# Optimization experiments

Hardware: AMD Instinct MI355X
Metric: run time of the kernel (lower is better)

Reference implementation:

```python
import jax, jax.numpy as jnp
import numpy as np


def setup_inputs() -> dict:
    key = jax.random.key(0)
    ks = jax.random.split(key, 5)
    B, S, D, U = 4, 2048, 1024, 1024
    scale = 1.0 / np.sqrt(D)
    return {
        "query": jax.random.normal(ks[0], (B, S, D), dtype=jnp.float32),
        "value": jax.random.normal(ks[1], (B, S, D), dtype=jnp.float32),
        "Wq": jax.random.normal(ks[2], (D, U), dtype=jnp.float32) * scale,
        "bq": jnp.zeros((U,), dtype=jnp.float32),
        "Wk": jax.random.normal(ks[3], (D, U), dtype=jnp.float32) * scale,
        "bk": jnp.zeros((U,), dtype=jnp.float32),
        "Wv": jax.random.normal(ks[4], (D, U), dtype=jnp.float32) * scale,
        "bv": jnp.zeros((U,), dtype=jnp.float32),
    }


def reference(query, value, Wq, bq, Wk, bk, Wv, bv):
    # Dense projections (last-dim matmul + bias)
    Q = jnp.einsum("bsd,du->bsu", query, Wq) + bq   # [B,Sq,U]
    K = jnp.einsum("btd,du->btu", value, Wk) + bk   # [B,Sk,U]
    V = jnp.einsum("btd,du->btu", value, Wv) + bv   # [B,Sk,U]
    d_k = jnp.asarray(K.shape[-1], dtype=jnp.float32)
    scores = jnp.einsum("bsu,btu->bst", Q, K) / jnp.sqrt(d_k)  # [B,Sq,Sk]
    weights = jax.nn.softmax(scores, axis=-1)
    return jnp.einsum("bst,btu->bsu", weights, V)   # [B,Sq,U]
```

## Files before the change

kernel.cpp:

```cpp
#include <hip/hip_runtime.h>
#include <hip/hip_bf16.h>
#include <stdint.h>

#define DEVINL __device__ __forceinline__

typedef __attribute__((ext_vector_type(4))) float f32x4;
typedef __attribute__((ext_vector_type(8))) __bf16 bfv8;
typedef __attribute__((ext_vector_type(8))) short s16x8;
typedef __attribute__((ext_vector_type(4))) short s16x4;

DEVINL short f2bf(float f) {
  union { float f; unsigned u; } v; v.f = f;
  unsigned r = v.u + 0x7FFFu + ((v.u >> 16) & 1u);
  return (short)(r >> 16);
}
DEVINL float bf2f(short h) {
  union { unsigned u; float f; } v; v.u = ((unsigned)(unsigned short)h) << 16;
  return v.f;
}
DEVINL void gload_lds16(const void* g, void* l) {
  __builtin_amdgcn_global_load_lds((__attribute__((address_space(1))) unsigned*)(g),
                                   (__attribute__((address_space(3))) unsigned*)(l),
                                   16, 0, 0);
}
#define S_BARRIER() __builtin_amdgcn_s_barrier()
#define LGKM0() asm volatile("s_waitcnt lgkmcnt(0)" ::: "memory")
#define MEMORD() asm volatile("" ::: "memory")
template <int N> DEVINL void vmwaitc() {
  asm volatile("s_waitcnt vmcnt(%0)" :: "i"(N) : "memory");
}

template <int BU, int NF>
DEVINL void gemm_core(const short* __restrict__ Ag, const short* __restrict__ Bg,
                      int lda, int ldb, int m0, int n0, int nkt,
                      short* lds, f32x4 (&acc)[8][NF]) {
  constexpr int U = 2 + BU;
  constexpr int SLOT = 8192 + BU * 4096;
  const int tid = threadIdx.x;
  const int w = tid >> 6, l = tid & 63;
  const int wm = w >> 2, wn = w & 3;
  const int lr = l & 15, lg = l >> 4;
  const int stg_row = w * 16 + (l >> 2);
  const int stg_col = (((l & 3) ^ ((l >> 3) & 3)) << 3);
  const int ck = ((lg ^ ((lr >> 1) & 3)) << 3);
  const int aro = (wm * 128 + lr) * 32 + ck;
  const int bro = 8192 + (wn * (NF * 16) + lr) * 32 + ck;
  const int dW = w * 512;

#pragma unroll
  for (int t = 0; t < 3; ++t) {
    short* S = lds + t * SLOT;
    gload_lds16(Ag + (size_t)(m0 + stg_row) * lda + t * 32 + stg_col, S + dW);
    gload_lds16(Ag + (size_t)(m0 + 128 + stg_row) * lda + t * 32 + stg_col, S + 4096 + dW);
#pragma unroll
    for (int u = 0; u < BU; ++u)
      gload_lds16(Bg + (size_t)(n0 + u * 128 + stg_row) * ldb + t * 32 + stg_col,
                  S + 8192 + u * 4096 + dW);
  }
  vmwaitc<2 * U>(); S_BARRIER(); MEMORD();

  bfv8 a[4], b[NF];
#pragma unroll 1
  for (int kt = 0; kt < nkt; ++kt) {
    const short* Sc = lds + (kt & 3) * SLOT;
    const int ks = kt + 3;
    short* Ss = lds + (ks & 3) * SLOT;
#pragma unroll
    for (int mf = 0; mf < 4; ++mf) a[mf] = *(const bfv8*)(Sc + aro + mf * 512);
#pragma unroll
    for (int nf = 0; nf < NF; ++nf) b[nf] = *(const bfv8*)(Sc + bro + nf * 512);
    if (ks < nkt) {
      gload_lds16(Ag + (size_t)(m0 + stg_row) * lda + ks * 32 + stg_col, Ss + dW);
      gload_lds16(Ag + (size_t)(m0 + 128 + stg_row) * lda + ks * 32 + stg_col, Ss + 4096 + dW);
    }
    S_BARRIER(); LGKM0();
    __builtin_amdgcn_s_setprio(1);
#pragma unroll
    for (int mf = 0; mf < 4; ++mf)
#pragma unroll
      for (int nf = 0; nf < NF; ++nf)
        acc[mf][nf] = __builtin_amdgcn_mfma_f32_16x16x32_bf16(a[mf], b[nf], acc[mf][nf], 0, 0, 0);
    __builtin_amdgcn_s_setprio(0);
    S_BARRIER(); MEMORD();
#pragma unroll
    for (int mf = 0; mf < 4; ++mf) a[mf] = *(const bfv8*)(Sc + aro + 2048 + mf * 512);
    if (ks < nkt) {
#pragma unroll
      for (int u = 0; u < BU; ++u)
        gload_lds16(Bg + (size_t)(n0 + u * 128 + stg_row) * ldb + ks * 32 + stg_col,
                    Ss + 8192 + u * 4096 + dW);
    }
    if (kt + 1 < nkt) {
      if (ks < nkt) vmwaitc<2 * U>();
      else if (kt + 2 < nkt) vmwaitc<U>();
      else vmwaitc<0>();
    }
    S_BARRIER(); LGKM0();
    __builtin_amdgcn_s_setprio(1);
#pragma unroll
    for (int mf = 0; mf < 4; ++mf)
#pragma unroll
      for (int nf = 0; nf < NF; ++nf)
        acc[4 + mf][nf] = __builtin_amdgcn_mfma_f32_16x16x32_bf16(a[mf], b[nf], acc[4 + mf][nf], 0, 0, 0);
    __builtin_amdgcn_s_setprio(0);
    S_BARRIER(); MEMORD();
  }
}

__global__ __launch_bounds__(256) void prep_kernel(
    const float* __restrict__ q, const float* __restrict__ v,
    const float* __restrict__ Wq, const float* __restrict__ Wk, const float* __restrict__ Wv,
    short* __restrict__ Qc, short* __restrict__ Vc,
    short* __restrict__ WTq, short* __restrict__ WTk, short* __restrict__ WTv) {
  __shared__ float tile[64][65];
  const int bx = blockIdx.x;
  if (bx < 8192) {
    const float* src = (bx < 4096) ? q : v;
    short* dst = (bx < 4096) ? Qc : Vc;
    const size_t i = ((size_t)(bx & 4095) * 256 + threadIdx.x) * 8;
    f32x4 x0 = *(const f32x4*)(src + i);
    f32x4 x1 = *(const f32x4*)(src + i + 4);
    s16x8 o;
#pragma unroll
    for (int j = 0; j < 4; ++j) { o[j] = f2bf(x0[j]); o[4 + j] = f2bf(x1[j]); }
    *(s16x8*)(dst + i) = o;
  } else {
    const int z = (bx - 8192) >> 8, xx = (bx - 8192) & 255;
    const float* W = (z == 0) ? Wq : (z == 1) ? Wk : Wv;
    short* WT = (z == 0) ? WTq : (z == 1) ? WTk : WTv;
    const int k0 = (xx & 15) << 6, n0 = (xx >> 4) << 6;
    const int c = threadIdx.x & 63, r0 = threadIdx.x >> 6;
#pragma unroll
    for (int i = 0; i < 16; ++i) {
      int r = (i << 2) + r0;
      tile[r][c] = W[(size_t)(k0 + r) * 1024 + n0 + c];
    }
    __syncthreads();
#pragma unroll
    for (int i = 0; i < 16; ++i) {
      int a = (i << 2) + r0;
      WT[(size_t)(n0 + a) * 1024 + k0 + c] = f2bf(tile[c][a]);
    }
  }
}

__global__ __launch_bounds__(512, 2) void qkproj_kernel(
    const short* __restrict__ Qc, const short* __restrict__ Vc,
    const short* __restrict__ WTq, const short* __restrict__ WTk,
    const float* __restrict__ bq, const float* __restrict__ bk,
    short* __restrict__ Qb, short* __restrict__ Kb) {
  __shared__ short lds[65536];
  const int bm = blockIdx.x >> 3, bn = blockIdx.x & 7;
  const int sel = bn >> 2;
  const short* A = sel ? Vc : Qc;
  const short* BT = sel ? WTk : WTq;
  const float* bias = sel ? bk : bq;
  short* O = sel ? Kb : Qb;
  const int m0 = bm * 256, n0 = (bn & 3) * 256;
  f32x4 acc[8][4];
#pragma unroll
  for (int i = 0; i < 8; ++i)
#pragma unroll
    for (int j = 0; j < 4; ++j) acc[i][j] = (f32x4){0.f, 0.f, 0.f, 0.f};
  gemm_core<2, 4>(A, BT, 1024, 1024, m0, n0, 32, lds, acc);
  const int tid = threadIdx.x;
  const int w = tid >> 6, l = tid & 63;
  const int wm = w >> 2, wn = w & 3, lr = l & 15, lg = l >> 4;
#pragma unroll
  for (int i = 0; i < 8; ++i) {
    const int row0 = m0 + wm * 128 + (i >> 2) * 64 + (i & 3) * 16 + lg * 4;
#pragma unroll
    for (int nf = 0; nf < 4; ++nf) {
      const int col = n0 + wn * 64 + nf * 16 + lr;
      const float bb = bias[col];
#pragma unroll
      for (int j = 0; j < 4; ++j)
        O[(size_t)(row0 + j) * 1024 + col] = f2bf(acc[i][nf][j] + bb);
    }
  }
}

__global__ __launch_bounds__(512, 2) void vproj_kernel(
    const short* __restrict__ Vc, const short* __restrict__ WTv,
    const float* __restrict__ bv, short* __restrict__ VT) {
  __shared__ short lds[49152];
  const int bm = blockIdx.x >> 3, bn = blockIdx.x & 7;
  const int m0 = bm * 256, n0 = bn * 128;
  f32x4 acc[8][2];
#pragma unroll
  for (int i = 0; i < 8; ++i)
#pragma unroll
    for (int j = 0; j < 2; ++j) acc[i][j] = (f32x4){0.f, 0.f, 0.f, 0.f};
  gemm_core<1, 2>(Vc, WTv, 1024, 1024, m0, n0, 32, lds, acc);
  const int tid = threadIdx.x;
  const int w = tid >> 6, l = tid & 63;
  const int wm = w >> 2, wn = w & 3, lr = l & 15, lg = l >> 4;
  __syncthreads();
#pragma unroll
  for (int i = 0; i < 8; ++i) {
    const int tl = wm * 128 + (i >> 2) * 64 + (i & 3) * 16 + lg * 4;
#pragma unroll
    for (int nf = 0; nf < 2; ++nf) {
      const int ul = wn * 32 + nf * 16 + lr;
      const float bb = bv[n0 + ul];
#pragma unroll
      for (int j = 0; j < 4; ++j)
        lds[ul * 264 + tl + j] = f2bf(acc[i][nf][j] + bb);
    }
  }
  __syncthreads();
  const int b = m0 >> 11, t0 = m0 & 2047;
#pragma unroll
  for (int it = 0; it < 8; ++it) {
    const int cid = it * 512 + tid;
    const int u = cid >> 5, tc = cid & 31;
    s16x8 v8 = *(const s16x8*)&lds[u * 264 + tc * 8];
    *(s16x8*)(VT + ((size_t)b * 1024 + n0 + u) * 2048 + t0 + tc * 8) = v8;
  }
}

__global__ __launch_bounds__(512, 2) void qkt8_kernel(const short* __restrict__ Qb,
                                                      const short* __restrict__ Kb,
                                                      short* __restrict__ Sb) {
  __shared__ short lds[65536];
  const int bt = blockIdx.y;
  const int bm = blockIdx.x >> 3, bn = blockIdx.x & 7;
  const short* A = Qb + (size_t)bt * 2097152;
  const short* B = Kb + (size_t)bt * 2097152;
  short* O = Sb + (size_t)bt * 4194304;
  const int m0 = bm * 256, n0 = bn * 256;
  f32x4 acc[8][4];
#pragma unroll
  for (int i = 0; i < 8; ++i)
#pragma unroll
    for (int j = 0; j < 4; ++j) acc[i][j] = (f32x4){0.f, 0.f, 0.f, 0.f};
  gemm_core<2, 4>(A, B, 1024, 1024, m0, n0, 32, lds, acc);
  const int tid = threadIdx.x;
  const int w = tid >> 6, l = tid & 63;
  const int wm = w >> 2, wn = w & 3, lr = l & 15, lg = l >> 4;
#pragma unroll
  for (int i = 0; i < 8; ++i) {
    const int row0 = m0 + wm * 128 + (i >> 2) * 64 + (i & 3) * 16 + lg * 4;
#pragma unroll
    for (int nf = 0; nf < 4; ++nf) {
      const int col = n0 + wn * 64 + nf * 16 + lr;
#pragma unroll
      for (int j = 0; j < 4; ++j)
        O[(size_t)(row0 + j) * 2048 + col] = f2bf(acc[i][nf][j] * 0.03125f);
    }
  }
}

__global__ __launch_bounds__(512, 2) void pv8_kernel(const short* __restrict__ Sb,
                                                     const short* __restrict__ VT,
                                                     float* __restrict__ Out) {
  __shared__ short lds[65536];
  const int bt = blockIdx.y;
  const int bm = blockIdx.x >> 2, bn = blockIdx.x & 3;
  const short* A = Sb + (size_t)bt * 4194304;
  const short* B = VT + (size_t)bt * 2097152;
  float* O = Out + (size_t)bt * 2097152;
  const int m0 = bm * 256, n0 = bn * 256;
  f32x4 acc[8][4];
#pragma unroll
  for (int i = 0; i < 8; ++i)
#pragma unroll
    for (int j = 0; j < 4; ++j) acc[i][j] = (f32x4){0.f, 0.f, 0.f, 0.f};
  gemm_core<2, 4>(A, B, 2048, 2048, m0, n0, 64, lds, acc);
  const int tid = threadIdx.x;
  const int w = tid >> 6, l = tid & 63;
  const int wm = w >> 2, wn = w & 3, lr = l & 15, lg = l >> 4;
#pragma unroll
  for (int i = 0; i < 8; ++i) {
    const int row0 = m0 + wm * 128 + (i >> 2) * 64 + (i & 3) * 16 + lg * 4;
#pragma unroll
    for (int nf = 0; nf < 4; ++nf) {
      const int col = n0 + wn * 64 + nf * 16 + lr;
#pragma unroll
      for (int j = 0; j < 4; ++j)
        O[(size_t)(row0 + j) * 1024 + col] = acc[i][nf][j];
    }
  }
}

__global__ __launch_bounds__(256) void softmax_kernel(short* __restrict__ Sb) {
  const size_t row = blockIdx.x;
  short* p = Sb + row * 2048;
  const int tid = threadIdx.x;
  const int w = tid >> 6, l = tid & 63;
  s16x8 v = *(const s16x8*)(p + tid * 8);
  float f[8];
#pragma unroll
  for (int j = 0; j < 8; ++j) f[j] = bf2f(v[j]);
  float m = f[0];
#pragma unroll
  for (int j = 1; j < 8; ++j) m = fmaxf(m, f[j]);
#pragma unroll
  for (int o = 32; o > 0; o >>= 1) m = fmaxf(m, __shfl_xor(m, o, 64));
  __shared__ float redm[4], reds[4];
  if (l == 0) redm[w] = m;
  __syncthreads();
  m = fmaxf(fmaxf(redm[0], redm[1]), fmaxf(redm[2], redm[3]));
  float s = 0.f;
#pragma unroll
  for (int j = 0; j < 8; ++j) { f[j] = __expf(f[j] - m); s += f[j]; }
#pragma unroll
  for (int o = 32; o > 0; o >>= 1) s += __shfl_xor(s, o, 64);
  if (l == 0) reds[w] = s;
  __syncthreads();
  s = reds[0] + reds[1] + reds[2] + reds[3];
  const float inv = 1.f / s;
  s16x8 o8;
#pragma unroll
  for (int j = 0; j < 8; ++j) o8[j] = f2bf(f[j] * inv);
  *(s16x8*)(p + tid * 8) = o8;
}

extern "C" void kernel_launch(void* const* d_in, const int* in_sizes, int n_in,
                              void* d_out, int out_size, void* d_ws, size_t ws_size,
                              hipStream_t stream) {
  const float* query = (const float*)d_in[0];
  const float* value = (const float*)d_in[1];
  const float* Wq = (const float*)d_in[2];
  const float* bq = (const float*)d_in[3];
  const float* Wk = (const float*)d_in[4];
  const float* bk = (const float*)d_in[5];
  const float* Wv = (const float*)d_in[6];
  const float* bv = (const float*)d_in[7];

  char* ws = (char*)d_ws;
  short* WTq = (short*)(ws);
  short* WTk = (short*)(ws + ((size_t)2 << 20));
  short* WTv = (short*)(ws + ((size_t)4 << 20));
  short* Qc  = (short*)(ws + ((size_t)6 << 20));
  short* Vc  = (short*)(ws + ((size_t)22 << 20));
  short* Sb  = (short*)(ws + ((size_t)6 << 20));
  short* Qb  = (short*)(ws + ((size_t)38 << 20));
  short* Kb  = (short*)(ws + ((size_t)54 << 20));
  short* VT  = (short*)(ws + ((size_t)70 << 20));

  prep_kernel<<<dim3(8960), 256, 0, stream>>>(query, value, Wq, Wk, Wv, Qc, Vc, WTq, WTk, WTv);

  qkproj_kernel<<<dim3(256), 512, 0, stream>>>(Qc, Vc, WTq, WTk, bq, bk, Qb, Kb);
  vproj_kernel<<<dim3(256), 512, 0, stream>>>(Vc, WTv, bv, VT);

  qkt8_kernel<<<dim3(64, 4), 512, 0, stream>>>(Qb, Kb, Sb);

  softmax_kernel<<<dim3(8192), 256, 0, stream>>>(Sb);

  pv8_kernel<<<dim3(32, 4), 512, 0, stream>>>(Sb, VT, (float*)d_out);
}
```

Measured before the change: 208.6 us.

## Replace LDS-pipelined GEMM core with direct-register 128x128 tiles and XCD swizzle

All four GEMM kernels now use a flat core that loads A/B fragments straight from global memory into registers with double-buffered register prefetch, instead of staging through LDS with a multi-stage async pipeline. Tiles shrink from 256x256 with 512 threads to 128x128 with 256 threads, raising the block count. Block indices are remapped so that consecutive blocks land on the same chiplet for L2 locality. This drops LDS usage and barriers, but every wave now refetches shared operand rows from cache, which adds global/L2 traffic and exposes load latency.

```diff
diff --git a/kernel.cpp b/kernel.cpp
--- a/kernel.cpp
+++ b/kernel.cpp
@@ -18,93 +18,49 @@
   union { unsigned u; float f; } v; v.u = ((unsigned)(unsigned short)h) << 16;
   return v.f;
 }
-DEVINL void gload_lds16(const void* g, void* l) {
-  __builtin_amdgcn_global_load_lds((__attribute__((address_space(1))) unsigned*)(g),
-                                   (__attribute__((address_space(3))) unsigned*)(l),
-                                   16, 0, 0);
-}
-#define S_BARRIER() __builtin_amdgcn_s_barrier()
-#define LGKM0() asm volatile("s_waitcnt lgkmcnt(0)" ::: "memory")
-#define MEMORD() asm volatile("" ::: "memory")
-template <int N> DEVINL void vmwaitc() {
-  asm volatile("s_waitcnt vmcnt(%0)" :: "i"(N) : "memory");
-}
-
-template <int BU, int NF>
-DEVINL void gemm_core(const short* __restrict__ Ag, const short* __restrict__ Bg,
-                      int lda, int ldb, int m0, int n0, int nkt,
-                      short* lds, f32x4 (&acc)[8][NF]) {
-  constexpr int U = 2 + BU;
-  constexpr int SLOT = 8192 + BU * 4096;
-  const int tid = threadIdx.x;
-  const int w = tid >> 6, l = tid & 63;
-  const int wm = w >> 2, wn = w & 3;
+DEVINL int xswz(int p, int n) { return (p & 7) * (n >> 3) + (p >> 3); }
+
+template <bool REFILL>
+DEVINL void step16(f32x4 (&acc)[4][4], bfv8 (&As)[4], bfv8 (&Bs)[4],
+                   const short* const (&pa)[4], const short* const (&pb)[4], int koff) {
+#pragma unroll
+  for (int mi = 0; mi < 4; ++mi) {
+#pragma unroll
+    for (int nf = 0; nf < 4; ++nf)
+      acc[mi][nf] = __builtin_amdgcn_mfma_f32_16x16x32_bf16(As[mi], Bs[nf], acc[mi][nf], 0, 0, 0);
+    if (REFILL) As[mi] = *(const bfv8*)(pa[mi] + koff * 32);
+  }
+  if (REFILL) {
+#pragma unroll
+    for (int nf = 0; nf < 4; ++nf) Bs[nf] = *(const bfv8*)(pb[nf] + koff * 32);
+  }
+}
+
+DEVINL void flat_core(const short* __restrict__ Ag, const short* __restrict__ Bg,
+                      int lda, int ldb, int m0, int n0, int nkt, f32x4 (&acc)[4][4]) {
+  const int l = threadIdx.x & 63, w = threadIdx.x >> 6;
+  const int wm = w >> 1, wn = w & 1;
   const int lr = l & 15, lg = l >> 4;
-  const int stg_row = w * 16 + (l >> 2);
-  const int stg_col = (((l & 3) ^ ((l >> 3) & 3)) << 3);
-  const int ck = ((lg ^ ((lr >> 1) & 3)) << 3);
-  const int aro = (wm * 128 + lr) * 32 + ck;
-  const int bro = 8192 + (wn * (NF * 16) + lr) * 32 + ck;
-  const int dW = w * 512;
-
-#pragma unroll
-  for (int t = 0; t < 3; ++t) {
-    short* S = lds + t * SLOT;
-    gload_lds16(Ag + (size_t)(m0 + stg_row) * lda + t * 32 + stg_col, S + dW);
-    gload_lds16(Ag + (size_t)(m0 + 128 + stg_row) * lda + t * 32 + stg_col, S + 4096 + dW);
-#pragma unroll
-    for (int u = 0; u < BU; ++u)
-      gload_lds16(Bg + (size_t)(n0 + u * 128 + stg_row) * ldb + t * 32 + stg_col,
-                  S + 8192 + u * 4096 + dW);
-  }
-  vmwaitc<2 * U>(); S_BARRIER(); MEMORD();
-
-  bfv8 a[4], b[NF];
+  const short* pa[4];
+  const short* pb[4];
+#pragma unroll
+  for (int i = 0; i < 4; ++i) {
+    pa[i] = Ag + (size_t)(m0 + wm * 64 + i * 16 + lr) * lda + lg * 8;
+    pb[i] = Bg + (size_t)(n0 + wn * 64 + i * 16 + lr) * ldb + lg * 8;
+  }
+  bfv8 a0[4], b0[4], a1[4], b1[4];
+#pragma unroll
+  for (int i = 0; i < 4; ++i) { a0[i] = *(const bfv8*)(pa[i]); b0[i] = *(const bfv8*)(pb[i]); }
+#pragma unroll
+  for (int i = 0; i < 4; ++i) { a1[i] = *(const bfv8*)(pa[i] + 32); b1[i] = *(const bfv8*)(pb[i] + 32); }
+  int kt = 0;
 #pragma unroll 1
-  for (int kt = 0; kt < nkt; ++kt) {
-    const short* Sc = lds + (kt & 3) * SLOT;
-    const int ks = kt + 3;
-    short* Ss = lds + (ks & 3) * SLOT;
-#pragma unroll
-    for (int mf = 0; mf < 4; ++mf) a[mf] = *(const bfv8*)(Sc + aro + mf * 512);
-#pragma unroll
-    for (int nf = 0; nf < NF; ++nf) b[nf] = *(const bfv8*)(Sc + bro + nf * 512);
-    if (ks < nkt) {
-      gload_lds16(Ag + (size_t)(m0 + stg_row) * lda + ks * 32 + stg_col, Ss + dW);
-      gload_lds16(Ag + (size_t)(m0 + 128 + stg_row) * lda + ks * 32 + stg_col, Ss + 4096 + dW);
-    }
-    S_BARRIER(); LGKM0();
-    __builtin_amdgcn_s_setprio(1);
-#pragma unroll
-    for (int mf = 0; mf < 4; ++mf)
-#pragma unroll
-      for (int nf = 0; nf < NF; ++nf)
-        acc[mf][nf] = __builtin_amdgcn_mfma_f32_16x16x32_bf16(a[mf], b[nf], acc[mf][nf], 0, 0, 0);
-    __builtin_amdgcn_s_setprio(0);
-    S_BARRIER(); MEMORD();
-#pragma unroll
-    for (int mf = 0; mf < 4; ++mf) a[mf] = *(const bfv8*)(Sc + aro + 2048 + mf * 512);
-    if (ks < nkt) {
-#pragma unroll
-      for (int u = 0; u < BU; ++u)
-        gload_lds16(Bg + (size_t)(n0 + u * 128 + stg_row) * ldb + ks * 32 + stg_col,
-                    Ss + 8192 + u * 4096 + dW);
-    }
-    if (kt + 1 < nkt) {
-      if (ks < nkt) vmwaitc<2 * U>();
-      else if (kt + 2 < nkt) vmwaitc<U>();
-      else vmwaitc<0>();
-    }
-    S_BARRIER(); LGKM0();
-    __builtin_amdgcn_s_setprio(1);
-#pragma unroll
-    for (int mf = 0; mf < 4; ++mf)
-#pragma unroll
-      for (int nf = 0; nf < NF; ++nf)
-        acc[4 + mf][nf] = __builtin_amdgcn_mfma_f32_16x16x32_bf16(a[mf], b[nf], acc[4 + mf][nf], 0, 0, 0);
-    __builtin_amdgcn_s_setprio(0);
-    S_BARRIER(); MEMORD();
-  }
+  for (; kt + 4 <= nkt; kt += 2) {
+    step16<true>(acc, a0, b0, pa, pb, kt + 2);
+    step16<true>(acc, a1, b1, pa, pb, kt + 3);
+  }
+  step16<false>(acc, a0, b0, pa, pb, 0);
+  step16<false>(acc, a1, b1, pa, pb, 0);
 }
 
 __global__ __launch_bounds__(256) void prep_kernel(
@@ -144,141 +100,139 @@
   }
 }
 
-__global__ __launch_bounds__(512, 2) void qkproj_kernel(
+__global__ __launch_bounds__(256, 2) void qkproj_kernel(
     const short* __restrict__ Qc, const short* __restrict__ Vc,
     const short* __restrict__ WTq, const short* __restrict__ WTk,
     const float* __restrict__ bq, const float* __restrict__ bk,
     short* __restrict__ Qb, short* __restrict__ Kb) {
-  __shared__ short lds[65536];
-  const int bm = blockIdx.x >> 3, bn = blockIdx.x & 7;
-  const int sel = bn >> 2;
+  const int o = xswz(blockIdx.x, 1024);
+  const int sel = o >> 9, r = o & 511;
+  const int bm = r >> 3, bn = r & 7;
   const short* A = sel ? Vc : Qc;
   const short* BT = sel ? WTk : WTq;
   const float* bias = sel ? bk : bq;
   short* O = sel ? Kb : Qb;
-  const int m0 = bm * 256, n0 = (bn & 3) * 256;
-  f32x4 acc[8][4];
-#pragma unroll
-  for (int i = 0; i < 8; ++i)
+  const int m0 = bm * 128, n0 = bn * 128;
+  f32x4 acc[4][4];
+#pragma unroll
+  for (int i = 0; i < 4; ++i)
 #pragma unroll
     for (int j = 0; j < 4; ++j) acc[i][j] = (f32x4){0.f, 0.f, 0.f, 0.f};
-  gemm_core<2, 4>(A, BT, 1024, 1024, m0, n0, 32, lds, acc);
-  const int tid = threadIdx.x;
-  const int w = tid >> 6, l = tid & 63;
-  const int wm = w >> 2, wn = w & 3, lr = l & 15, lg = l >> 4;
-#pragma unroll
-  for (int i = 0; i < 8; ++i) {
-    const int row0 = m0 + wm * 128 + (i >> 2) * 64 + (i & 3) * 16 + lg * 4;
+  flat_core(A, BT, 1024, 1024, m0, n0, 32, acc);
+  const int l = threadIdx.x & 63, w = threadIdx.x >> 6;
+  const int wm = w >> 1, wn = w & 1, lr = l & 15, lg = l >> 4;
+#pragma unroll
+  for (int mi = 0; mi < 4; ++mi) {
+    const int row0 = m0 + wm * 64 + mi * 16 + lg * 4;
 #pragma unroll
     for (int nf = 0; nf < 4; ++nf) {
       const int col = n0 + wn * 64 + nf * 16 + lr;
       const float bb = bias[col];
 #pragma unroll
       for (int j = 0; j < 4; ++j)
-        O[(size_t)(row0 + j) * 1024 + col] = f2bf(acc[i][nf][j] + bb);
-    }
-  }
-}
-
-__global__ __launch_bounds__(512, 2) void vproj_kernel(
+        O[(size_t)(row0 + j) * 1024 + col] = f2bf(acc[mi][nf][j] + bb);
+    }
+  }
+}
+
+__global__ __launch_bounds__(256, 2) void vproj_kernel(
     const short* __restrict__ Vc, const short* __restrict__ WTv,
     const float* __restrict__ bv, short* __restrict__ VT) {
-  __shared__ short lds[49152];
-  const int bm = blockIdx.x >> 3, bn = blockIdx.x & 7;
-  const int m0 = bm * 256, n0 = bn * 128;
-  f32x4 acc[8][2];
-#pragma unroll
-  for (int i = 0; i < 8; ++i)
-#pragma unroll
-    for (int j = 0; j < 2; ++j) acc[i][j] = (f32x4){0.f, 0.f, 0.f, 0.f};
-  gemm_core<1, 2>(Vc, WTv, 1024, 1024, m0, n0, 32, lds, acc);
+  __shared__ short lt[128 * 136];
+  const int o = xswz(blockIdx.x, 512);
+  const int bm = o >> 3, bn = o & 7;
+  const int m0 = bm * 128, n0 = bn * 128;
+  f32x4 acc[4][4];
+#pragma unroll
+  for (int i = 0; i < 4; ++i)
+#pragma unroll
+    for (int j = 0; j < 4; ++j) acc[i][j] = (f32x4){0.f, 0.f, 0.f, 0.f};
+  flat_core(Vc, WTv, 1024, 1024, m0, n0, 32, acc);
   const int tid = threadIdx.x;
-  const int w = tid >> 6, l = tid & 63;
-  const int wm = w >> 2, wn = w & 3, lr = l & 15, lg = l >> 4;
-  __syncthreads();
-#pragma unroll
-  for (int i = 0; i < 8; ++i) {
-    const int tl = wm * 128 + (i >> 2) * 64 + (i & 3) * 16 + lg * 4;
-#pragma unroll
-    for (int nf = 0; nf < 2; ++nf) {
-      const int ul = wn * 32 + nf * 16 + lr;
+  const int l = tid & 63, w = tid >> 6;
+  const int wm = w >> 1, wn = w & 1, lr = l & 15, lg = l >> 4;
+#pragma unroll
+  for (int mi = 0; mi < 4; ++mi) {
+    const int tl = wm * 64 + mi * 16 + lg * 4;
+#pragma unroll
+    for (int nf = 0; nf < 4; ++nf) {
+      const int ul = wn * 64 + nf * 16 + lr;
       const float bb = bv[n0 + ul];
-#pragma unroll
-      for (int j = 0; j < 4; ++j)
-        lds[ul * 264 + tl + j] = f2bf(acc[i][nf][j] + bb);
+      s16x4 pk;
+#pragma unroll
+      for (int j = 0; j < 4; ++j) pk[j] = f2bf(acc[mi][nf][j] + bb);
+      *(s16x4*)&lt[ul * 136 + tl] = pk;
     }
   }
   __syncthreads();
   const int b = m0 >> 11, t0 = m0 & 2047;
 #pragma unroll
   for (int it = 0; it < 8; ++it) {
-    const int cid = it * 512 + tid;
-    const int u = cid >> 5, tc = cid & 31;
-    s16x8 v8 = *(const s16x8*)&lds[u * 264 + tc * 8];
+    const int cid = it * 256 + tid;
+    const int u = cid >> 4, tc = cid & 15;
+    s16x8 v8 = *(const s16x8*)&lt[u * 136 + tc * 8];
     *(s16x8*)(VT + ((size_t)b * 1024 + n0 + u) * 2048 + t0 + tc * 8) = v8;
   }
 }
 
-__global__ __launch_bounds__(512, 2) void qkt8_kernel(const short* __restrict__ Qb,
-                                                      const short* __restrict__ Kb,
-                                                      short* __restrict__ Sb) {
-  __shared__ short lds[65536];
-  const int bt = blockIdx.y;
-  const int bm = blockIdx.x >> 3, bn = blockIdx.x & 7;
+__global__ __launch_bounds__(256, 2) void qkt_kernel(const short* __restrict__ Qb,
+                                                     const short* __restrict__ Kb,
+                                                     short* __restrict__ Sb) {
+  const int o = xswz(blockIdx.x, 1024);
+  const int bt = o >> 8, r = o & 255;
+  const int bm = r >> 4, bn = r & 15;
   const short* A = Qb + (size_t)bt * 2097152;
   const short* B = Kb + (size_t)bt * 2097152;
   short* O = Sb + (size_t)bt * 4194304;
-  const int m0 = bm * 256, n0 = bn * 256;
-  f32x4 acc[8][4];
-#pragma unroll
-  for (int i = 0; i < 8; ++i)
+  const int m0 = bm * 128, n0 = bn * 128;
+  f32x4 acc[4][4];
+#pragma unroll
+  for (int i = 0; i < 4; ++i)
 #pragma unroll
     for (int j = 0; j < 4; ++j) acc[i][j] = (f32x4){0.f, 0.f, 0.f, 0.f};
-  gemm_core<2, 4>(A, B, 1024, 1024, m0, n0, 32, lds, acc);
-  const int tid = threadIdx.x;
-  const int w = tid >> 6, l = tid & 63;
-  const int wm = w >> 2, wn = w & 3, lr = l & 15, lg = l >> 4;
-#pragma unroll
-  for (int i = 0; i < 8; ++i) {
-    const int row0 = m0 + wm * 128 + (i >> 2) * 64 + (i & 3) * 16 + lg * 4;
+  flat_core(A, B, 1024, 1024, m0, n0, 32, acc);
+  const int l = threadIdx.x & 63, w = threadIdx.x >> 6;
+  const int wm = w >> 1, wn = w & 1, lr = l & 15, lg = l >> 4;
+#pragma unroll
+  for (int mi = 0; mi < 4; ++mi) {
+    const int row0 = m0 + wm * 64 + mi * 16 + lg * 4;
 #pragma unroll
     for (int nf = 0; nf < 4; ++nf) {
       const int col = n0 + wn * 64 + nf * 16 + lr;
 #pragma unroll
       for (int j = 0; j < 4; ++j)
-        O[(size_t)(row0 + j) * 2048 + col] = f2bf(acc[i][nf][j] * 0.03125f);
-    }
-  }
-}
-
-__global__ __launch_bounds__(512, 2) void pv8_kernel(const short* __restrict__ Sb,
-                                                     const short* __restrict__ VT,
-                                                     float* __restrict__ Out) {
-  __shared__ short lds[65536];
-  const int bt = blockIdx.y;
-  const int bm = blockIdx.x >> 2, bn = blockIdx.x & 3;
+        O[(size_t)(row0 + j) * 2048 + col] = f2bf(acc[mi][nf][j] * 0.03125f);
+    }
+  }
+}
+
+__global__ __launch_bounds__(256, 2) void pv_kernel(const short* __restrict__ Sb,
+                                                    const short* __restrict__ VT,
+                                                    float* __restrict__ Out) {
+  const int o = xswz(blockIdx.x, 512);
+  const int bt = o >> 7, r = o & 127;
+  const int bm = r >> 3, bn = r & 7;
   const short* A = Sb + (size_t)bt * 4194304;
   const short* B = VT + (size_t)bt * 2097152;
   float* O = Out + (size_t)bt * 2097152;
-  const int m0 = bm * 256, n0 = bn * 256;
-  f32x4 acc[8][4];
-#pragma unroll
-  for (int i = 0; i < 8; ++i)
+  const int m0 = bm * 128, n0 = bn * 128;
+  f32x4 acc[4][4];
+#pragma unroll
+  for (int i = 0; i < 4; ++i)
 #pragma unroll
     for (int j = 0; j < 4; ++j) acc[i][j] = (f32x4){0.f, 0.f, 0.f, 0.f};
-  gemm_core<2, 4>(A, B, 2048, 2048, m0, n0, 64, lds, acc);
-  const int tid = threadIdx.x;
-  const int w = tid >> 6, l = tid & 63;
-  const int wm = w >> 2, wn = w & 3, lr = l & 15, lg = l >> 4;
-#pragma unroll
-  for (int i = 0; i < 8; ++i) {
-    const int row0 = m0 + wm * 128 + (i >> 2) * 64 + (i & 3) * 16 + lg * 4;
+  flat_core(A, B, 2048, 2048, m0, n0, 64, acc);
+  const int l = threadIdx.x & 63, w = threadIdx.x >> 6;
+  const int wm = w >> 1, wn = w & 1, lr = l & 15, lg = l >> 4;
+#pragma unroll
+  for (int mi = 0; mi < 4; ++mi) {
+    const int row0 = m0 + wm * 64 + mi * 16 + lg * 4;
 #pragma unroll
     for (int nf = 0; nf < 4; ++nf) {
       const int col = n0 + wn * 64 + nf * 16 + lr;
 #pragma unroll
       for (int j = 0; j < 4; ++j)
-        O[(size_t)(row0 + j) * 1024 + col] = acc[i][nf][j];
+        O[(size_t)(row0 + j) * 1024 + col] = acc[mi][nf][j];
     }
   }
 }
@@ -341,12 +295,12 @@
 
   prep_kernel<<<dim3(8960), 256, 0, stream>>>(query, value, Wq, Wk, Wv, Qc, Vc, WTq, WTk, WTv);
 
-  qkproj_kernel<<<dim3(256), 512, 0, stream>>>(Qc, Vc, WTq, WTk, bq, bk, Qb, Kb);
-  vproj_kernel<<<dim3(256), 512, 0, stream>>>(Vc, WTv, bv, VT);
-
-  qkt8_kernel<<<dim3(64, 4), 512, 0, stream>>>(Qb, Kb, Sb);
+  qkproj_kernel<<<dim3(1024), 256, 0, stream>>>(Qc, Vc, WTq, WTk, bq, bk, Qb, Kb);
+  vproj_kernel<<<dim3(512), 256, 0, stream>>>(Vc, WTv, bv, VT);
+
+  qkt_kernel<<<dim3(1024), 256, 0, stream>>>(Qb, Kb, Sb);
 
   softmax_kernel<<<dim3(8192), 256, 0, stream>>>(Sb);
 
-  pv8_kernel<<<dim3(32, 4), 512, 0, stream>>>(Sb, VT, (float*)d_out);
-}
+  pv_kernel<<<dim3(512), 256, 0, stream>>>(Sb, VT, (float*)d_out);
+}
```

Result: slower. 442.6 us (+112.2%).

## Shrink GEMM tiles to 256x128, use 3-slot LDS ring, swizzle block order

Applied to the files above, without the earlier changes.

Makes the pipeline depth of the shared GEMM core a template parameter and moves all GEMMs to a 3-stage ring with 256x128 tiles, which lowers LDS per block so qkproj and qkt can run four blocks per CU. Grids double, and block indices are remapped with an XCD-style swizzle so neighbouring tiles share L2. The V-projection epilogue now packs four bf16 values per LDS store. The aim is better occupancy and wave balance across the CUs, at the cost of lower per-block data reuse and a shallower prefetch.

```diff
diff --git a/kernel.cpp b/kernel.cpp
--- a/kernel.cpp
+++ b/kernel.cpp
@@ -29,13 +29,15 @@
 template <int N> DEVINL void vmwaitc() {
   asm volatile("s_waitcnt vmcnt(%0)" :: "i"(N) : "memory");
 }
-
-template <int BU, int NF>
+DEVINL int xswz(int p, int n) { return (p & 7) * (n >> 3) + (p >> 3); }
+
+template <int BU, int NF, int RING>
 DEVINL void gemm_core(const short* __restrict__ Ag, const short* __restrict__ Bg,
                       int lda, int ldb, int m0, int n0, int nkt,
                       short* lds, f32x4 (&acc)[8][NF]) {
   constexpr int U = 2 + BU;
   constexpr int SLOT = 8192 + BU * 4096;
+  constexpr int WS = (RING - 2) * U;
   const int tid = threadIdx.x;
   const int w = tid >> 6, l = tid & 63;
   const int wm = w >> 2, wn = w & 3;
@@ -48,7 +50,7 @@
   const int dW = w * 512;
 
 #pragma unroll
-  for (int t = 0; t < 3; ++t) {
+  for (int t = 0; t < RING - 1; ++t) {
     short* S = lds + t * SLOT;
     gload_lds16(Ag + (size_t)(m0 + stg_row) * lda + t * 32 + stg_col, S + dW);
     gload_lds16(Ag + (size_t)(m0 + 128 + stg_row) * lda + t * 32 + stg_col, S + 4096 + dW);
@@ -57,14 +59,15 @@
       gload_lds16(Bg + (size_t)(n0 + u * 128 + stg_row) * ldb + t * 32 + stg_col,
                   S + 8192 + u * 4096 + dW);
   }
-  vmwaitc<2 * U>(); S_BARRIER(); MEMORD();
-
+  vmwaitc<WS>(); S_BARRIER(); MEMORD();
+
+  int cur = 0, stg = RING - 1;
   bfv8 a[4], b[NF];
 #pragma unroll 1
   for (int kt = 0; kt < nkt; ++kt) {
-    const short* Sc = lds + (kt & 3) * SLOT;
-    const int ks = kt + 3;
-    short* Ss = lds + (ks & 3) * SLOT;
+    const short* Sc = lds + cur * SLOT;
+    short* Ss = lds + stg * SLOT;
+    const int ks = kt + (RING - 1);
 #pragma unroll
     for (int mf = 0; mf < 4; ++mf) a[mf] = *(const bfv8*)(Sc + aro + mf * 512);
 #pragma unroll
@@ -91,7 +94,7 @@
                     Ss + 8192 + u * 4096 + dW);
     }
     if (kt + 1 < nkt) {
-      if (ks < nkt) vmwaitc<2 * U>();
+      if (ks < nkt) vmwaitc<WS>();
       else if (kt + 2 < nkt) vmwaitc<U>();
       else vmwaitc<0>();
     }
@@ -104,6 +107,8 @@
         acc[4 + mf][nf] = __builtin_amdgcn_mfma_f32_16x16x32_bf16(a[mf], b[nf], acc[4 + mf][nf], 0, 0, 0);
     __builtin_amdgcn_s_setprio(0);
     S_BARRIER(); MEMORD();
+    cur = (cur + 1 == RING) ? 0 : cur + 1;
+    stg = (stg + 1 == RING) ? 0 : stg + 1;
   }
 }
 
@@ -144,25 +149,26 @@
   }
 }
 
-__global__ __launch_bounds__(512, 2) void qkproj_kernel(
+__global__ __launch_bounds__(512, 4) void qkproj_kernel(
     const short* __restrict__ Qc, const short* __restrict__ Vc,
     const short* __restrict__ WTq, const short* __restrict__ WTk,
     const float* __restrict__ bq, const float* __restrict__ bk,
     short* __restrict__ Qb, short* __restrict__ Kb) {
-  __shared__ short lds[65536];
-  const int bm = blockIdx.x >> 3, bn = blockIdx.x & 7;
-  const int sel = bn >> 2;
+  __shared__ short lds[36864];
+  const int o = xswz(blockIdx.x, 512);
+  const int sel = o >> 8, r = o & 255;
+  const int bm = r >> 3, bn = r & 7;
   const short* A = sel ? Vc : Qc;
   const short* BT = sel ? WTk : WTq;
   const float* bias = sel ? bk : bq;
   short* O = sel ? Kb : Qb;
-  const int m0 = bm * 256, n0 = (bn & 3) * 256;
-  f32x4 acc[8][4];
+  const int m0 = bm * 256, n0 = bn * 128;
+  f32x4 acc[8][2];
 #pragma unroll
   for (int i = 0; i < 8; ++i)
 #pragma unroll
-    for (int j = 0; j < 4; ++j) acc[i][j] = (f32x4){0.f, 0.f, 0.f, 0.f};
-  gemm_core<2, 4>(A, BT, 1024, 1024, m0, n0, 32, lds, acc);
+    for (int j = 0; j < 2; ++j) acc[i][j] = (f32x4){0.f, 0.f, 0.f, 0.f};
+  gemm_core<1, 2, 3>(A, BT, 1024, 1024, m0, n0, 32, lds, acc);
   const int tid = threadIdx.x;
   const int w = tid >> 6, l = tid & 63;
   const int wm = w >> 2, wn = w & 3, lr = l & 15, lg = l >> 4;
@@ -170,8 +176,8 @@
   for (int i = 0; i < 8; ++i) {
     const int row0 = m0 + wm * 128 + (i >> 2) * 64 + (i & 3) * 16 + lg * 4;
 #pragma unroll
-    for (int nf = 0; nf < 4; ++nf) {
-      const int col = n0 + wn * 64 + nf * 16 + lr;
+    for (int nf = 0; nf < 2; ++nf) {
+      const int col = n0 + wn * 32 + nf * 16 + lr;
       const float bb = bias[col];
 #pragma unroll
       for (int j = 0; j < 4; ++j)
@@ -183,19 +189,21 @@
 __global__ __launch_bounds__(512, 2) void vproj_kernel(
     const short* __restrict__ Vc, const short* __restrict__ WTv,
     const float* __restrict__ bv, short* __restrict__ VT) {
-  __shared__ short lds[49152];
-  const int bm = blockIdx.x >> 3, bn = blockIdx.x & 7;
+  __shared__ short lds[36864];
+  const int o = xswz(blockIdx.x, 256);
+  const int bm = o >> 3, bn = o & 7;
   const int m0 = bm * 256, n0 = bn * 128;
   f32x4 acc[8][2];
 #pragma unroll
   for (int i = 0; i < 8; ++i)
 #pragma unroll
     for (int j = 0; j < 2; ++j) acc[i][j] = (f32x4){0.f, 0.f, 0.f, 0.f};
-  gemm_core<1, 2>(Vc, WTv, 1024, 1024, m0, n0, 32, lds, acc);
+  gemm_core<1, 2, 3>(Vc, WTv, 1024, 1024, m0, n0, 32, lds, acc);
   const int tid = threadIdx.x;
   const int w = tid >> 6, l = tid & 63;
   const int wm = w >> 2, wn = w & 3, lr = l & 15, lg = l >> 4;
   __syncthreads();
+  short* lt = lds;
 #pragma unroll
   for (int i = 0; i < 8; ++i) {
     const int tl = wm * 128 + (i >> 2) * 64 + (i & 3) * 16 + lg * 4;
@@ -203,9 +211,10 @@
     for (int nf = 0; nf < 2; ++nf) {
       const int ul = wn * 32 + nf * 16 + lr;
       const float bb = bv[n0 + ul];
-#pragma unroll
-      for (int j = 0; j < 4; ++j)
-        lds[ul * 264 + tl + j] = f2bf(acc[i][nf][j] + bb);
+      s16x4 pk;
+#pragma unroll
+      for (int j = 0; j < 4; ++j) pk[j] = f2bf(acc[i][nf][j] + bb);
+      *(s16x4*)&lt[ul * 264 + tl] = pk;
     }
   }
   __syncthreads();
@@ -214,27 +223,28 @@
   for (int it = 0; it < 8; ++it) {
     const int cid = it * 512 + tid;
     const int u = cid >> 5, tc = cid & 31;
-    s16x8 v8 = *(const s16x8*)&lds[u * 264 + tc * 8];
+    s16x8 v8 = *(const s16x8*)&lt[u * 264 + tc * 8];
     *(s16x8*)(VT + ((size_t)b * 1024 + n0 + u) * 2048 + t0 + tc * 8) = v8;
   }
 }
 
-__global__ __launch_bounds__(512, 2) void qkt8_kernel(const short* __restrict__ Qb,
-                                                      const short* __restrict__ Kb,
-                                                      short* __restrict__ Sb) {
-  __shared__ short lds[65536];
-  const int bt = blockIdx.y;
-  const int bm = blockIdx.x >> 3, bn = blockIdx.x & 7;
+__global__ __launch_bounds__(512, 4) void qkt_kernel(const short* __restrict__ Qb,
+                                                     const short* __restrict__ Kb,
+                                                     short* __restrict__ Sb) {
+  __shared__ short lds[36864];
+  const int o = xswz(blockIdx.x, 512);
+  const int bt = o >> 7, r = o & 127;
+  const int bm = r >> 4, bn = r & 15;
   const short* A = Qb + (size_t)bt * 2097152;
   const short* B = Kb + (size_t)bt * 2097152;
   short* O = Sb + (size_t)bt * 4194304;
-  const int m0 = bm * 256, n0 = bn * 256;
-  f32x4 acc[8][4];
+  const int m0 = bm * 256, n0 = bn * 128;
+  f32x4 acc[8][2];
 #pragma unroll
   for (int i = 0; i < 8; ++i)
 #pragma unroll
-    for (int j = 0; j < 4; ++j) acc[i][j] = (f32x4){0.f, 0.f, 0.f, 0.f};
-  gemm_core<2, 4>(A, B, 1024, 1024, m0, n0, 32, lds, acc);
+    for (int j = 0; j < 2; ++j) acc[i][j] = (f32x4){0.f, 0.f, 0.f, 0.f};
+  gemm_core<1, 2, 3>(A, B, 1024, 1024, m0, n0, 32, lds, acc);
   const int tid = threadIdx.x;
   const int w = tid >> 6, l = tid & 63;
   const int wm = w >> 2, wn = w & 3, lr = l & 15, lg = l >> 4;
@@ -242,8 +252,8 @@
   for (int i = 0; i < 8; ++i) {
     const int row0 = m0 + wm * 128 + (i >> 2) * 64 + (i & 3) * 16 + lg * 4;
 #pragma unroll
-    for (int nf = 0; nf < 4; ++nf) {
-      const int col = n0 + wn * 64 + nf * 16 + lr;
+    for (int nf = 0; nf < 2; ++nf) {
+      const int col = n0 + wn * 32 + nf * 16 + lr;
 #pragma unroll
       for (int j = 0; j < 4; ++j)
         O[(size_t)(row0 + j) * 2048 + col] = f2bf(acc[i][nf][j] * 0.03125f);
@@ -251,31 +261,31 @@
   }
 }
 
-__global__ __launch_bounds__(512, 2) void pv8_kernel(const short* __restrict__ Sb,
-                                                     const short* __restrict__ VT,
-                                                     float* __restrict__ Out) {
-  __shared__ short lds[65536];
-  const int bt = blockIdx.y;
-  const int bm = blockIdx.x >> 2, bn = blockIdx.x & 3;
+__global__ __launch_bounds__(512, 2) void pv_kernel(const short* __restrict__ Sb,
+                                                    const short* __restrict__ VT,
+                                                    float* __restrict__ Out) {
+  __shared__ short lds[36864];
+  const int o = xswz(blockIdx.x, 256);
+  const int bt = o >> 6, r = o & 63;
+  const int bm = r >> 3, bn = r & 7;
   const short* A = Sb + (size_t)bt * 4194304;
   const short* B = VT + (size_t)bt * 2097152;
   float* O = Out + (size_t)bt * 2097152;
-  const int m0 = bm * 256, n0 = bn * 256;
-  f32x4 acc[8][4];
+  const int m0 = bm * 256, n0 = bn * 128;
+  f32x4 acc[8][2];
 #pragma unroll
   for (int i = 0; i < 8; ++i)
 #pragma unroll
-    for (int j = 0; j < 4; ++j) acc[i][j] = (f32x4){0.f, 0.f, 0.f, 0.f};
-  gemm_core<2, 4>(A, B, 2048, 2048, m0, n0, 64, lds, acc);
-  const int tid = threadIdx.x;
-  const int w = tid >> 6, l = tid & 63;
+    for (int j = 0; j < 2; ++j) acc[i][j] = (f32x4){0.f, 0.f, 0.f, 0.f};
+  gemm_core<1, 2, 3>(A, B, 2048, 2048, m0, n0, 64, lds, acc);
+  const int l = threadIdx.x & 63, w = threadIdx.x >> 6;
   const int wm = w >> 2, wn = w & 3, lr = l & 15, lg = l >> 4;
 #pragma unroll
   for (int i = 0; i < 8; ++i) {
     const int row0 = m0 + wm * 128 + (i >> 2) * 64 + (i & 3) * 16 + lg * 4;
 #pragma unroll
-    for (int nf = 0; nf < 4; ++nf) {
-      const int col = n0 + wn * 64 + nf * 16 + lr;
+    for (int nf = 0; nf < 2; ++nf) {
+      const int col = n0 + wn * 32 + nf * 16 + lr;
 #pragma unroll
       for (int j = 0; j < 4; ++j)
         O[(size_t)(row0 + j) * 1024 + col] = acc[i][nf][j];
@@ -341,12 +351,12 @@
 
   prep_kernel<<<dim3(8960), 256, 0, stream>>>(query, value, Wq, Wk, Wv, Qc, Vc, WTq, WTk, WTv);
 
-  qkproj_kernel<<<dim3(256), 512, 0, stream>>>(Qc, Vc, WTq, WTk, bq, bk, Qb, Kb);
+  qkproj_kernel<<<dim3(512), 512, 0, stream>>>(Qc, Vc, WTq, WTk, bq, bk, Qb, Kb);
   vproj_kernel<<<dim3(256), 512, 0, stream>>>(Vc, WTv, bv, VT);
 
-  qkt8_kernel<<<dim3(64, 4), 512, 0, stream>>>(Qb, Kb, Sb);
+  qkt_kernel<<<dim3(512), 512, 0, stream>>>(Qb, Kb, Sb);
 
   softmax_kernel<<<dim3(8192), 256, 0, stream>>>(Sb);
 
-  pv8_kernel<<<dim3(32, 4), 512, 0, stream>>>(Sb, VT, (float*)d_out);
-}
+  pv_kernel<<<dim3(256), 512, 0, stream>>>(Sb, VT, (float*)d_out);
+}
```

Result: faster. 193.0 us (-7.5%).
